# Kernel tuning notes

Measured on AMD Instinct MI355X. Metric: run time of the kernel, lower is better.

Reference implementation:

```python
import jax, jax.numpy as jnp
import numpy as np
import math

B, C, N, T = 8, 128, 256, 64  # batch, d_model, nodes, timesteps
H = 8                          # attention heads
NUM_STEPS = 50                 # diffusion steps


def _conv2d(x, w, b):
    # Conv2d with kernel (1,3), padding (0,1); x: (B,C,N,T), w: (O,I,1,3)
    y = jax.lax.conv_general_dilated(x, w, (1, 1), [(0, 0), (1, 1)],
                                     dimension_numbers=('NCHW', 'OIHW', 'NCHW'))
    return y + b[None, :, None, None]


def _linear(x, w, b=None):
    y = jnp.einsum('...i,oi->...o', x, w)
    return y if b is None else y + b


def _ln(x, g, b, eps=1e-5):
    m = jnp.mean(x, -1, keepdims=True)
    v = jnp.var(x, -1, keepdims=True)
    return (x - m) * jax.lax.rsqrt(v + eps) * g + b


def _forward(step, x, adj, wq, bq, wk, bk, w1, b1, w2, b2, theta,
             ln0_g, ln0_b, ln1_g, ln1_b, p1_w, p1_b, p2_w, p2_b,
             dxc_w, dxc_b, dec_w, dec_b, dc1_w, dc1_b, dp2_w, dp2_b):
    dk = C // H
    sq = 1.0 / math.sqrt(dk)
    sc = 1.0 / math.sqrt(C)
    # ---- normalized graph Laplacian: D^{-1/2} A D^{-1/2} (get_laplacian, normalize=True)
    d = jnp.sum(adj, -1) ** -0.5
    Lap = adj * d[:, None] * d[None, :]  # (N,N)
    # ---- temporal attention with conv-derived Q/K (MultiHeadAttentionAwareTemporal)
    q = _conv2d(x, wq, bq).reshape(B, H, dk, N, T).transpose(0, 3, 1, 4, 2)  # (B,N,H,T,dk)
    k = _conv2d(x, wk, bk).reshape(B, H, dk, N, T).transpose(0, 3, 1, 4, 2)
    v = _linear(x.transpose(0, 2, 3, 1), w1, b1).reshape(B, N, T, H, dk).transpose(0, 1, 3, 2, 4)
    p = jax.nn.softmax(jnp.einsum('bnhtd,bnhsd->bnhts', q, k) * sq, axis=-1)
    o = jnp.einsum('bnhts,bnhsd->bnhtd', p, v).transpose(0, 1, 3, 2, 4).reshape(B, N, T, C)
    xp = x.transpose(0, 2, 3, 1) + _ln(_linear(o, w2, b2), ln0_g, ln0_b)  # (B,N,T,C)
    # ---- spatial attention GCN (Spatial_Attention_layer + spatialAttentionGCN)
    xt = xp.transpose(0, 2, 1, 3)  # (B,T,N,C)
    sat = jax.nn.softmax(jnp.einsum('btnf,btmf->btnm', xt, xt) * sc, axis=-1) * sc
    y = jnp.einsum('btnm,btmf->btnf', Lap[None, None] * sat, xt)
    y = jax.nn.relu(_linear(y, theta)).transpose(0, 2, 1, 3)  # (B,N,T,C)
    h = xp + _ln(y, ln1_g, ln1_b)
    # ---- diffusion step embedding (DiffusionEmbedding)
    dim = C // 2
    freqs = 10.0 ** (jnp.arange(dim, dtype=jnp.float32) / (dim - 1) * 4.0)
    tab = jnp.arange(NUM_STEPS, dtype=jnp.float32)[:, None] * freqs[None, :]
    tab = jnp.concatenate([jnp.sin(tab), jnp.cos(tab)], -1)  # (NUM_STEPS, C)
    e = jax.nn.silu(_linear(tab[step], p1_w, p1_b))
    e = jax.nn.silu(_linear(e, p2_w, p2_b))  # (B,C)
    h = h + e[:, None, None, :]
    # ---- Decoder: conv + sigmoid-gated add + relu + 1x1 projection to 2 channels
    enc = h.transpose(0, 3, 1, 2)  # (B,C,N,T)
    xh = _conv2d(enc, dxc_w, dxc_b)
    ec = _conv2d(enc, dec_w, dec_b)
    out = jax.nn.relu(xh + jax.nn.sigmoid(ec) + _conv2d(ec, dc1_w, dc1_b))
    out = jnp.einsum('bcnt,oc->bont', out, dp2_w) + dp2_b[None, :, None, None]  # (B,2,N,T)
    return out


def setup_inputs() -> dict:
    key = jax.random.key(0)
    ks = iter(jax.random.split(key, 40))
    s = 1.0 / math.sqrt(C)
    sk = 1.0 / math.sqrt(3 * C)

    def nrm(shape, scale):
        return jax.random.normal(next(ks), shape, jnp.float32) * scale

    return {
        'x': nrm((B, C, N, T), 1.0),
        'adj': jax.random.uniform(next(ks), (N, N), jnp.float32, 0.1, 1.0),
        'step': jax.random.randint(next(ks), (B,), 0, NUM_STEPS, jnp.int32),
        'wq': nrm((C, C, 1, 3), sk), 'bq': jnp.zeros((C,), jnp.float32),
        'wk': nrm((C, C, 1, 3), sk), 'bk': jnp.zeros((C,), jnp.float32),
        'w1': nrm((C, C), s), 'b1': jnp.zeros((C,), jnp.float32),
        'w2': nrm((C, C), s), 'b2': jnp.zeros((C,), jnp.float32),
        'theta': nrm((C, C), s),
        'ln0_g': jnp.ones((C,), jnp.float32), 'ln0_b': jnp.zeros((C,), jnp.float32),
        'ln1_g': jnp.ones((C,), jnp.float32), 'ln1_b': jnp.zeros((C,), jnp.float32),
        'p1_w': nrm((C, C), s), 'p1_b': jnp.zeros((C,), jnp.float32),
        'p2_w': nrm((C, C), s), 'p2_b': jnp.zeros((C,), jnp.float32),
        'dxc_w': nrm((C, C, 1, 3), sk), 'dxc_b': jnp.zeros((C,), jnp.float32),
        'dec_w': nrm((C, C, 1, 3), sk), 'dec_b': jnp.zeros((C,), jnp.float32),
        'dc1_w': nrm((C, C, 1, 3), sk), 'dc1_b': jnp.zeros((C,), jnp.float32),
        'dp2_w': nrm((2, C), s), 'dp2_b': jnp.zeros((2,), jnp.float32),
    }


def reference(x, adj, step, wq, bq, wk, bk, w1, b1, w2, b2, theta,
              ln0_g, ln0_b, ln1_g, ln1_b, p1_w, p1_b, p2_w, p2_b,
              dxc_w, dxc_b, dec_w, dec_b, dc1_w, dc1_b, dp2_w, dp2_b):
    return _forward(step, x, adj, wq, bq, wk, bk, w1, b1, w2, b2, theta,
                    ln0_g, ln0_b, ln1_g, ln1_b, p1_w, p1_b, p2_w, p2_b,
                    dxc_w, dxc_b, dec_w, dec_b, dc1_w, dc1_b, dp2_w, dp2_b)
```

## Files before the change

### kernel.cpp

```cpp
#include <hip/hip_runtime.h>
#include <hip/hip_bf16.h>

namespace {

constexpr int C = 128, N = 256, T = 64, Bsz = 8;
constexpr int TILE = T * C;
constexpr size_t BIGE = (size_t)Bsz * N * T * C;

typedef short v8s __attribute__((ext_vector_type(8)));
typedef float v4f __attribute__((ext_vector_type(4)));

__device__ __forceinline__ float bfu(unsigned short u) {
  unsigned int x = ((unsigned int)u) << 16;
  return __uint_as_float(x);
}
__device__ __forceinline__ unsigned short f2b(float v) {
  __hip_bfloat16 h = __float2bfloat16(v);
  return *(unsigned short*)&h;
}
__device__ __forceinline__ unsigned int pk2(float a, float b) {
  return (unsigned int)f2b(a) | ((unsigned int)f2b(b) << 16);
}
__device__ __forceinline__ float ld(const void* p, size_t i, int f32) {
  if (f32) return ((const float*)p)[i];
  return bfu(((const unsigned short*)p)[i]);
}
__device__ __forceinline__ float sigm(float x) { return 1.f / (1.f + __expf(-x)); }

__global__ __launch_bounds__(64) void k_sniff(const unsigned short* x, int* flag) {
  __shared__ int cnt[64];
  int tid = threadIdx.x;
  int c = 0;
  for (int u = 0; u < 8; ++u) {
    unsigned short v = x[tid * 8 + u];
    int e = (v >> 7) & 255;
    c += (e >= 97 && e <= 157) ? 1 : 0;
  }
  cnt[tid] = c;
  __syncthreads();
  if (tid == 0) {
    int s = 0;
    for (int i = 0; i < 64; ++i) s += cnt[i];
    flag[0] = (s < 435) ? 1 : 0;
  }
}

struct PrepArgs {
  const int* flag;
  const void *wq, *wk, *w1, *w2, *th, *dxc, *dec, *dc1;
  const void *bq, *bk, *b1, *b2, *l0g, *l0b, *l1g, *l1b, *dxcb, *decb, *dc1b, *dp2w, *dp2b;
  unsigned short *wqkB, *w1B, *w2B;
  __hip_bfloat16* thB;
  unsigned short *decWb, *dxcWb, *dc1Wb;
  float *bqk, *b1f, *b2f, *l0gf, *l0bf, *l1gf, *l1bf, *dxcbf, *decbf, *dc1bf, *dp2wf, *dp2bf;
};

__global__ __launch_bounds__(256) void k_prepall(
    PrepArgs a, const void* adj, float* lap, const int* step,
    const void* p1w, const void* p1b, const void* p2w, const void* p2b, float* e) {
  __shared__ float sh[256];
  __shared__ float e1[128];
  int f = a.flag[0];
  int blk = blockIdx.x, tid = threadIdx.x;
  if (blk < 128) {
    int idx = blk * 256 + tid;
    const int stride = 32768;
    for (int i = idx; i < 256 * 384; i += stride) {
      int o = i / 384, k = i - o * 384;
      int j = k >> 7, ii = k & 127;
      float v = (o < 128) ? ld(a.wq, (o * 128 + ii) * 3 + j, f)
                          : ld(a.wk, ((o - 128) * 128 + ii) * 3 + j, f);
      a.wqkB[i] = f2b(v);
    }
    for (int i = idx; i < 16384; i += stride) {
      a.w1B[i] = f2b(ld(a.w1, i, f));
      a.w2B[i] = f2b(ld(a.w2, i, f));
      a.thB[i] = __float2bfloat16(ld(a.th, i, f));
    }
    for (int i = idx; i < 16384; i += stride) {
      int o = i >> 7, ii = i & 127;
      int sbase = (o * 128 + ii) * 3;
#pragma unroll
      for (int j = 0; j < 3; ++j) {
        int dsti = o * 384 + j * 128 + ii;
        a.decWb[dsti] = f2b(ld(a.dec, sbase + j, f));
        a.dxcWb[dsti] = f2b(ld(a.dxc, sbase + j, f));
        a.dc1Wb[dsti] = f2b(ld(a.dc1, sbase + j, f));
      }
    }
    for (int i = idx; i < 256; i += stride) {
      a.bqk[i] = (i < 128) ? ld(a.bq, i, f) : ld(a.bk, i - 128, f);
      a.dp2wf[i] = ld(a.dp2w, i, f);
    }
    for (int i = idx; i < 128; i += stride) {
      a.b1f[i] = ld(a.b1, i, f);   a.b2f[i] = ld(a.b2, i, f);
      a.l0gf[i] = ld(a.l0g, i, f); a.l0bf[i] = ld(a.l0b, i, f);
      a.l1gf[i] = ld(a.l1g, i, f); a.l1bf[i] = ld(a.l1b, i, f);
      a.dxcbf[i] = ld(a.dxcb, i, f); a.decbf[i] = ld(a.decb, i, f); a.dc1bf[i] = ld(a.dc1b, i, f);
    }
    if (idx < 2) a.dp2bf[idx] = ld(a.dp2b, idx, f);
  } else if (blk < 192) {
    float s = 0.f;
    for (int m = 0; m < 256; ++m) s += ld(adj, tid * 256 + m, f);
    sh[tid] = 1.f / sqrtf(s);
    __syncthreads();
    int n0 = (blk - 128) * 4;
    for (int idx = tid; idx < 1024; idx += 256) {
      int n = n0 + (idx >> 8), m = idx & 255;
      lap[n * 256 + m] = ld(adj, n * 256 + m, f) * sh[n] * sh[m];
    }
  } else {
    int b = blk - 192;
    if (tid < 128) {
      float sv = (float)step[b];
      int i0 = tid & 63;
      float fr = powf(10.f, (float)i0 / 63.f * 4.f);
      float ang = sv * fr;
      sh[tid] = (tid < 64) ? sinf(ang) : cosf(ang);
    }
    __syncthreads();
    if (tid < 128) {
      float aa = ld(p1b, tid, f);
      for (int i = 0; i < 128; ++i) aa += sh[i] * ld(p1w, tid * 128 + i, f);
      aa = aa * sigm(aa);
      e1[tid] = aa;
    }
    __syncthreads();
    if (tid < 128) {
      float a2 = ld(p2b, tid, f);
      for (int i = 0; i < 128; ++i) a2 += e1[i] * ld(p2w, tid * 128 + i, f);
      e[b * 128 + tid] = a2 * sigm(a2);
    }
  }
}

constexpr int XBS = 136;
constexpr int VTS = 72;

__global__ __launch_bounds__(512, 4) void k_mega1(
    const void* xin, const int* flag,
    const unsigned short* wqkB, const float* bqk,
    const unsigned short* w1B, const float* b1f,
    const unsigned short* w2B, const float* b2f,
    const float* l0g, const float* l0b, float* g0) {
  int bn = blockIdx.x, b = bn >> 8, n = bn & 255;
  __shared__ unsigned short Xb[66 * XBS];
  __shared__ unsigned short qo[64 * XBS];
  __shared__ unsigned short kls[64 * XBS];
  __shared__ unsigned short vT[128 * VTS];
  __shared__ float pS[8 * 64], pQ[8 * 64];
  __shared__ float mrow[64], vrow[64];
  int tid = threadIdx.x;
  int wv = tid >> 6, lane = tid & 63, quad = lane >> 4, lr = lane & 15;
  int f = flag[0];
  int hb = wv * 16;
  const v8s zz = {0, 0, 0, 0, 0, 0, 0, 0};
  {
    size_t xoff = (size_t)b * C * N * T + (size_t)n * T;
    const int NT = N * T;
    for (int idx = tid; idx < 1024; idx += 512) {
      int t = idx & 63, c0 = (idx >> 6) * 8;
      union { unsigned short us[8]; uint4 q; } pk;
      if (f) {
        const float* xp = (const float*)xin + xoff + (size_t)c0 * NT + t;
#pragma unroll
        for (int u = 0; u < 8; ++u) pk.us[u] = f2b(xp[(size_t)u * NT]);
      } else {
        const unsigned short* xp = (const unsigned short*)xin + xoff + (size_t)c0 * NT + t;
#pragma unroll
        for (int u = 0; u < 8; ++u) pk.us[u] = xp[(size_t)u * NT];
      }
      *(uint4*)&Xb[(t + 1) * XBS + c0] = pk.q;
    }
    if (tid < 128) { Xb[tid] = 0; Xb[65 * XBS + tid] = 0; }
  }
  __syncthreads();
  {
    int mt0 = wv * 2;
    v4f acc[2][4];
#pragma unroll
    for (int mi = 0; mi < 2; ++mi)
#pragma unroll
      for (int nt = 0; nt < 4; ++nt) acc[mi][nt] = (v4f){0.f, 0.f, 0.f, 0.f};
    for (int j = 0; j < 3; ++j) {
#pragma unroll
      for (int kt = 0; kt < 4; ++kt) {
        int ko = j * 128 + kt * 32 + quad * 8;
        v8s a0 = *(const v8s*)&wqkB[(mt0 * 16 + lr) * 384 + ko];
        v8s a1 = *(const v8s*)&wqkB[((mt0 + 1) * 16 + lr) * 384 + ko];
        int bko = kt * 32 + quad * 8;
#pragma unroll
        for (int nt = 0; nt < 4; ++nt) {
          v8s bb = *(const v8s*)&Xb[(nt * 16 + lr + j) * XBS + bko];
          acc[0][nt] = __builtin_amdgcn_mfma_f32_16x16x32_bf16(a0, bb, acc[0][nt], 0, 0, 0);
          acc[1][nt] = __builtin_amdgcn_mfma_f32_16x16x32_bf16(a1, bb, acc[1][nt], 0, 0, 0);
        }
      }
    }
    unsigned short* dst = (wv < 4) ? qo : kls;
#pragma unroll
    for (int mi = 0; mi < 2; ++mi) {
      int og = (mt0 + mi) * 16 + quad * 4;
      int oo = og & 127;
#pragma unroll
      for (int nt = 0; nt < 4; ++nt) {
        int t = nt * 16 + lr;
        *(unsigned int*)&dst[t * XBS + oo] =
            pk2(acc[mi][nt][0] + bqk[og], acc[mi][nt][1] + bqk[og + 1]);
        *(unsigned int*)&dst[t * XBS + oo + 2] =
            pk2(acc[mi][nt][2] + bqk[og + 2], acc[mi][nt][3] + bqk[og + 3]);
      }
    }
  }
  {
    v4f av[4];
#pragma unroll
    for (int nt = 0; nt < 4; ++nt) av[nt] = (v4f){0.f, 0.f, 0.f, 0.f};
#pragma unroll
    for (int kt = 0; kt < 4; ++kt) {
      int ko = kt * 32 + quad * 8;
      v8s a = *(const v8s*)&w1B[(wv * 16 + lr) * 128 + ko];
#pragma unroll
      for (int nt = 0; nt < 4; ++nt) {
        v8s bb = *(const v8s*)&Xb[(nt * 16 + lr + 1) * XBS + ko];
        av[nt] = __builtin_amdgcn_mfma_f32_16x16x32_bf16(a, bb, av[nt], 0, 0, 0);
      }
    }
#pragma unroll
    for (int nt = 0; nt < 4; ++nt) {
      int t = nt * 16 + lr;
#pragma unroll
      for (int r = 0; r < 4; ++r) {
        int o = hb + quad * 4 + r;
        vT[o * VTS + t] = f2b(av[nt][r] + b1f[o]);
      }
    }
  }
  __syncthreads();
  {
    v4f sa[4][4];
#pragma unroll
    for (int ms = 0; ms < 4; ++ms)
#pragma unroll
      for (int nt = 0; nt < 4; ++nt) sa[ms][nt] = (v4f){0.f, 0.f, 0.f, 0.f};
    {
      v8s afs[4], bfs[4];
#pragma unroll
      for (int ms = 0; ms < 4; ++ms)
        afs[ms] = (quad < 2) ? *(const v8s*)&kls[(ms * 16 + lr) * XBS + hb + quad * 8] : zz;
#pragma unroll
      for (int nt = 0; nt < 4; ++nt)
        bfs[nt] = (quad < 2) ? *(const v8s*)&qo[(nt * 16 + lr) * XBS + hb + quad * 8] : zz;
#pragma unroll
      for (int ms = 0; ms < 4; ++ms)
#pragma unroll
        for (int nt = 0; nt < 4; ++nt)
          sa[ms][nt] = __builtin_amdgcn_mfma_f32_16x16x32_bf16(afs[ms], bfs[nt], sa[ms][nt], 0, 0, 0);
    }
#pragma unroll
    for (int nt = 0; nt < 4; ++nt) {
      float mx = -1e30f;
#pragma unroll
      for (int ms = 0; ms < 4; ++ms)
#pragma unroll
        for (int r = 0; r < 4; ++r) {
          float v = sa[ms][nt][r] * 0.25f;
          sa[ms][nt][r] = v;
          mx = fmaxf(mx, v);
        }
      mx = fmaxf(mx, __shfl_xor(mx, 16, 64));
      mx = fmaxf(mx, __shfl_xor(mx, 32, 64));
      float ssum = 0.f;
#pragma unroll
      for (int ms = 0; ms < 4; ++ms)
#pragma unroll
        for (int r = 0; r < 4; ++r) {
          float e = __expf(sa[ms][nt][r] - mx);
          sa[ms][nt][r] = e;
          ssum += e;
        }
      ssum += __shfl_xor(ssum, 16, 64);
      ssum += __shfl_xor(ssum, 32, 64);
      float inv = 1.f / ssum;
#pragma unroll
      for (int ms = 0; ms < 4; ++ms)
#pragma unroll
        for (int r = 0; r < 4; ++r) sa[ms][nt][r] *= inv;
    }
    v4f ov[4];
#pragma unroll
    for (int nt = 0; nt < 4; ++nt) ov[nt] = (v4f){0.f, 0.f, 0.f, 0.f};
#pragma unroll
    for (int kt = 0; kt < 2; ++kt) {
      unsigned int pA[4][2], pB[4][2];
#pragma unroll
      for (int nt = 0; nt < 4; ++nt) {
#pragma unroll
        for (int h = 0; h < 2; ++h) {
          pA[nt][h] = pk2(sa[2 * kt][nt][2 * h], sa[2 * kt][nt][2 * h + 1]);
          pB[nt][h] = pk2(sa[2 * kt + 1][nt][2 * h], sa[2 * kt + 1][nt][2 * h + 1]);
        }
      }
      v8s aV = *(const v8s*)&vT[(hb + lr) * VTS + kt * 32 + quad * 8];
#pragma unroll
      for (int nt = 0; nt < 4; ++nt) {
        union { unsigned int u[4]; v8s s; } bu;
#pragma unroll
        for (int w = 0; w < 4; ++w) {
          int src = (2 * (quad & 1) + (w >> 1)) * 16 + lr;
          unsigned int x0 = (unsigned int)__shfl((int)pA[nt][w & 1], src, 64);
          unsigned int x1 = (unsigned int)__shfl((int)pB[nt][w & 1], src, 64);
          bu.u[w] = (quad >> 1) ? x1 : x0;
        }
        ov[nt] = __builtin_amdgcn_mfma_f32_16x16x32_bf16(aV, bu.s, ov[nt], 0, 0, 0);
      }
    }
#pragma unroll
    for (int nt = 0; nt < 4; ++nt) {
      int t = nt * 16 + lr;
      *(unsigned int*)&qo[t * XBS + hb + quad * 4] = pk2(ov[nt][0], ov[nt][1]);
      *(unsigned int*)&qo[t * XBS + hb + quad * 4 + 2] = pk2(ov[nt][2], ov[nt][3]);
    }
  }
  __syncthreads();
  v4f aw[4];
  {
#pragma unroll
    for (int nt = 0; nt < 4; ++nt) aw[nt] = (v4f){0.f, 0.f, 0.f, 0.f};
#pragma unroll
    for (int kt = 0; kt < 4; ++kt) {
      int ko = kt * 32 + quad * 8;
      v8s a = *(const v8s*)&w2B[(wv * 16 + lr) * 128 + ko];
#pragma unroll
      for (int nt = 0; nt < 4; ++nt) {
        v8s bb = *(const v8s*)&qo[(nt * 16 + lr) * XBS + ko];
        aw[nt] = __builtin_amdgcn_mfma_f32_16x16x32_bf16(a, bb, aw[nt], 0, 0, 0);
      }
    }
    int ob = hb + quad * 4;
#pragma unroll
    for (int nt = 0; nt < 4; ++nt) {
      float s = 0.f, q2 = 0.f;
#pragma unroll
      for (int r = 0; r < 4; ++r) {
        aw[nt][r] += b2f[ob + r];
        s += aw[nt][r];
        q2 += aw[nt][r] * aw[nt][r];
      }
      s += __shfl_xor(s, 16, 64);  s += __shfl_xor(s, 32, 64);
      q2 += __shfl_xor(q2, 16, 64); q2 += __shfl_xor(q2, 32, 64);
      if (quad == 0) {
        pS[wv * 64 + nt * 16 + lr] = s;
        pQ[wv * 64 + nt * 16 + lr] = q2;
      }
    }
  }
  __syncthreads();
  if (tid < 64) {
    float s = 0.f, q2 = 0.f;
#pragma unroll
    for (int w = 0; w < 8; ++w) { s += pS[w * 64 + tid]; q2 += pQ[w * 64 + tid]; }
    float mm = s * (1.f / 128.f);
    mrow[tid] = mm;
    vrow[tid] = rsqrtf(q2 * (1.f / 128.f) - mm * mm + 1e-5f);
  }
  __syncthreads();
  {
    int ob = hb + quad * 4;
    float gg[4], bb2[4];
#pragma unroll
    for (int r = 0; r < 4; ++r) { gg[r] = l0g[ob + r]; bb2[r] = l0b[ob + r]; }
    float* dst = g0 + (size_t)bn * TILE;
#pragma unroll
    for (int nt = 0; nt < 4; ++nt) {
      int t = nt * 16 + lr;
      float m = mrow[t], rs = vrow[t];
      ushort4 xr = *(const ushort4*)&Xb[(t + 1) * XBS + ob];
      float4 o4;
      o4.x = (aw[nt][0] - m) * rs * gg[0] + bb2[0] + bfu(xr.x);
      o4.y = (aw[nt][1] - m) * rs * gg[1] + bb2[1] + bfu(xr.y);
      o4.z = (aw[nt][2] - m) * rs * gg[2] + bb2[2] + bfu(xr.z);
      o4.w = (aw[nt][3] - m) * rs * gg[3] + bb2[3] + bfu(xr.w);
      *(float4*)&dst[t * 128 + ob] = o4;
    }
  }
}

constexpr int XS = 136;
constexpr int TS = 264;

__global__ __launch_bounds__(512, 1) void k_megasp(
    const float* g0, const float* lap, const unsigned short* thB,
    const float* l1g, const float* l1b, const float* e, unsigned short* g0b) {
  int bt = blockIdx.x, b = bt >> 6, t = bt & 63;
  __shared__ unsigned short R1[256 * XS];
  __shared__ unsigned short R2[256 * XS];
  __shared__ float pS[8][256], pQ[8][256];
  __shared__ float mrow[256], vrow[256];
  unsigned short* Xhi = R1;
  unsigned short* Xlo = R2;
  unsigned short* Xt = R2;
  unsigned short* Pld = R1;
  int tid = threadIdx.x;
  int wv = tid >> 6, lane = tid & 63, quad = lane >> 4, lr = lane & 15;
  int wrow0 = wv * 32;
  const float sc = 0.08838834764831845f;
  {
    size_t base = (size_t)b * (N * (size_t)TILE) + (size_t)t * 128;
    for (int idx = tid * 4; idx < 32768; idx += 2048) {
      int n = idx >> 7, c = idx & 127;
      float4 v4 = *(const float4*)&g0[base + (size_t)n * TILE + c];
      ushort4 h, l;
      h.x = f2b(v4.x); l.x = f2b(v4.x - bfu(h.x));
      h.y = f2b(v4.y); l.y = f2b(v4.y - bfu(h.y));
      h.z = f2b(v4.z); l.z = f2b(v4.z - bfu(h.z));
      h.w = f2b(v4.w); l.w = f2b(v4.w - bfu(h.w));
      *(ushort4*)&Xhi[n * XS + c] = h;
      *(ushort4*)&Xlo[n * XS + c] = l;
    }
  }
  __syncthreads();
  v4f acc[2][16];
#pragma unroll
  for (int mi = 0; mi < 2; ++mi)
#pragma unroll
    for (int nt = 0; nt < 16; ++nt) acc[mi][nt] = (v4f){0.f, 0.f, 0.f, 0.f};
  for (int kt = 0; kt < 4; ++kt) {
    int ko = kt * 32 + quad * 8;
    v8s ah0 = *(const v8s*)&Xhi[(wrow0 + lr) * XS + ko];
    v8s al0 = *(const v8s*)&Xlo[(wrow0 + lr) * XS + ko];
    v8s ah1 = *(const v8s*)&Xhi[(wrow0 + 16 + lr) * XS + ko];
    v8s al1 = *(const v8s*)&Xlo[(wrow0 + 16 + lr) * XS + ko];
#pragma unroll
    for (int nt = 0; nt < 16; ++nt) {
      v8s bh = *(const v8s*)&Xhi[(nt * 16 + lr) * XS + ko];
      v8s bl = *(const v8s*)&Xlo[(nt * 16 + lr) * XS + ko];
      acc[0][nt] = __builtin_amdgcn_mfma_f32_16x16x32_bf16(ah0, bh, acc[0][nt], 0, 0, 0);
      acc[0][nt] = __builtin_amdgcn_mfma_f32_16x16x32_bf16(ah0, bl, acc[0][nt], 0, 0, 0);
      acc[0][nt] = __builtin_amdgcn_mfma_f32_16x16x32_bf16(al0, bh, acc[0][nt], 0, 0, 0);
      acc[1][nt] = __builtin_amdgcn_mfma_f32_16x16x32_bf16(ah1, bh, acc[1][nt], 0, 0, 0);
      acc[1][nt] = __builtin_amdgcn_mfma_f32_16x16x32_bf16(ah1, bl, acc[1][nt], 0, 0, 0);
      acc[1][nt] = __builtin_amdgcn_mfma_f32_16x16x32_bf16(al1, bh, acc[1][nt], 0, 0, 0);
    }
  }
  __syncthreads();
  for (int task = tid; task < 8192; task += 512) {
    int c = task & 127, n0 = (task >> 7) * 4;
    ushort4 w;
    w.x = Xhi[(n0 + 0) * XS + c];
    w.y = Xhi[(n0 + 1) * XS + c];
    w.z = Xhi[(n0 + 2) * XS + c];
    w.w = Xhi[(n0 + 3) * XS + c];
    *(ushort4*)&Xt[c * TS + n0] = w;
  }
  __syncthreads();
  unsigned int pk1[2][8][2];
#pragma unroll
  for (int mi = 0; mi < 2; ++mi) {
#pragma unroll
    for (int r = 0; r < 4; ++r) {
      int row = wrow0 + 16 * mi + quad * 4 + r;
      float mx = -1e30f;
#pragma unroll
      for (int nt = 0; nt < 16; ++nt) {
        acc[mi][nt][r] *= sc;
        mx = fmaxf(mx, acc[mi][nt][r]);
      }
#pragma unroll
      for (int m = 8; m > 0; m >>= 1) mx = fmaxf(mx, __shfl_xor(mx, m, 16));
      float ex[16];
      float ssum = 0.f;
#pragma unroll
      for (int nt = 0; nt < 16; ++nt) { ex[nt] = __expf(acc[mi][nt][r] - mx); ssum += ex[nt]; }
#pragma unroll
      for (int m = 8; m > 0; m >>= 1) ssum += __shfl_xor(ssum, m, 16);
      float inv = sc / ssum;
      const float* lrow = lap + row * 256 + lr;
#pragma unroll
      for (int nt = 0; nt < 8; ++nt)
        Pld[row * XS + nt * 16 + lr] = f2b(ex[nt] * inv * lrow[nt * 16]);
#pragma unroll
      for (int nt = 8; nt < 16; ++nt) {
        unsigned int hbw = (unsigned int)f2b(ex[nt] * inv * lrow[nt * 16]);
        if ((r & 1) == 0) pk1[mi][nt - 8][r >> 1] = hbw;
        else pk1[mi][nt - 8][r >> 1] |= hbw << 16;
      }
    }
  }
  v4f acc2[2][8];
#pragma unroll
  for (int mi = 0; mi < 2; ++mi)
#pragma unroll
    for (int nt = 0; nt < 8; ++nt) acc2[mi][nt] = (v4f){0.f, 0.f, 0.f, 0.f};
#pragma unroll
  for (int h = 0; h < 2; ++h) {
    if (h == 1) {
#pragma unroll
      for (int mi = 0; mi < 2; ++mi) {
        int rowb = wrow0 + 16 * mi + quad * 4;
#pragma unroll
        for (int k = 0; k < 8; ++k) {
          int col = k * 16 + lr;
          unsigned int u0 = pk1[mi][k][0], u1 = pk1[mi][k][1];
          Pld[(rowb + 0) * XS + col] = (unsigned short)u0;
          Pld[(rowb + 1) * XS + col] = (unsigned short)(u0 >> 16);
          Pld[(rowb + 2) * XS + col] = (unsigned short)u1;
          Pld[(rowb + 3) * XS + col] = (unsigned short)(u1 >> 16);
        }
      }
    }
    for (int kt = 0; kt < 4; ++kt) {
      int ko = kt * 32 + quad * 8;
      v8s pa0 = *(const v8s*)&Pld[(wrow0 + lr) * XS + ko];
      v8s pa1 = *(const v8s*)&Pld[(wrow0 + 16 + lr) * XS + ko];
#pragma unroll
      for (int nt = 0; nt < 8; ++nt) {
        v8s xb = *(const v8s*)&Xt[(nt * 16 + lr) * TS + h * 128 + ko];
        acc2[0][nt] = __builtin_amdgcn_mfma_f32_16x16x32_bf16(pa0, xb, acc2[0][nt], 0, 0, 0);
        acc2[1][nt] = __builtin_amdgcn_mfma_f32_16x16x32_bf16(pa1, xb, acc2[1][nt], 0, 0, 0);
      }
    }
  }
  __syncthreads();
  unsigned short* yB = R2;
  unsigned short* ths = R1;
#pragma unroll
  for (int mi = 0; mi < 2; ++mi) {
    int nb = wrow0 + 16 * mi + quad * 4;
#pragma unroll
    for (int nt = 0; nt < 8; ++nt) {
      int c = nt * 16 + lr;
#pragma unroll
      for (int r = 0; r < 4; ++r)
        yB[(nb + r) * XS + c] = f2b(acc2[mi][nt][r]);
    }
  }
  for (int idx = tid * 8; idx < 16384; idx += 4096) {
    int o = idx >> 7, k = idx & 127;
    *(uint4*)&ths[o * 136 + k] = *(const uint4*)&thB[idx];
  }
  __syncthreads();
  v4f acc3[16];
#pragma unroll
  for (int nt = 0; nt < 16; ++nt) acc3[nt] = (v4f){0.f, 0.f, 0.f, 0.f};
#pragma unroll
  for (int kt = 0; kt < 4; ++kt) {
    int ko = kt * 32 + quad * 8;
    v8s a = *(const v8s*)&ths[(wv * 16 + lr) * 136 + ko];
#pragma unroll
    for (int nt = 0; nt < 16; ++nt) {
      v8s bb = *(const v8s*)&yB[(nt * 16 + lr) * XS + ko];
      acc3[nt] = __builtin_amdgcn_mfma_f32_16x16x32_bf16(a, bb, acc3[nt], 0, 0, 0);
    }
  }
#pragma unroll
  for (int nt = 0; nt < 16; ++nt) {
    float s = 0.f, q2 = 0.f;
#pragma unroll
    for (int r = 0; r < 4; ++r) {
      float v = fmaxf(acc3[nt][r], 0.f);
      acc3[nt][r] = v;
      s += v; q2 += v * v;
    }
    s += __shfl_xor(s, 16, 64);  s += __shfl_xor(s, 32, 64);
    q2 += __shfl_xor(q2, 16, 64); q2 += __shfl_xor(q2, 32, 64);
    if (quad == 0) { pS[wv][nt * 16 + lr] = s; pQ[wv][nt * 16 + lr] = q2; }
  }
  __syncthreads();
  if (tid < 256) {
    float s = 0.f, q2 = 0.f;
#pragma unroll
    for (int w = 0; w < 8; ++w) { s += pS[w][tid]; q2 += pQ[w][tid]; }
    float mm = s * (1.f / 128.f);
    mrow[tid] = mm;
    vrow[tid] = rsqrtf(q2 * (1.f / 128.f) - mm * mm + 1e-5f);
  }
  __syncthreads();
  {
    int o0 = wv * 16 + quad * 4;
    float gg[4], bb2[4], ev[4];
    const float* eb = e + b * 128;
#pragma unroll
    for (int r = 0; r < 4; ++r) { gg[r] = l1g[o0 + r]; bb2[r] = l1b[o0 + r]; ev[r] = eb[o0 + r]; }
#pragma unroll
    for (int nt = 0; nt < 16; ++nt) {
      int n = nt * 16 + lr;
      float m = mrow[n], rs = vrow[n];
      size_t ga = ((size_t)(b * 256 + n)) * TILE + (size_t)t * 128 + o0;
      float4 xa = *(const float4*)&g0[ga];
      ushort4 pk;
      pk.x = f2b((acc3[nt][0] - m) * rs * gg[0] + bb2[0] + xa.x + ev[0]);
      pk.y = f2b((acc3[nt][1] - m) * rs * gg[1] + bb2[1] + xa.y + ev[1]);
      pk.z = f2b((acc3[nt][2] - m) * rs * gg[2] + bb2[2] + xa.z + ev[2]);
      pk.w = f2b((acc3[nt][3] - m) * rs * gg[3] + bb2[3] + xa.w + ev[3]);
      *(ushort4*)&g0b[ga] = pk;
    }
  }
}

__global__ __launch_bounds__(512, 4) void k_megadec(
    const unsigned short* g0b, const unsigned short* decW, const float* decb,
    const unsigned short* dxcW, const float* dxcb,
    const unsigned short* dc1W, const float* dc1b,
    const float* dp2w, const float* dp2b, const int* flag, void* outv) {
  int bn = blockIdx.x, b = bn >> 8, n = bn & 255;
  int f32o = flag[0];
  __shared__ unsigned short Xm[66 * XBS];
  __shared__ unsigned short E2[66 * XBS];
  __shared__ float pb0[8][64], pb1[8][64];
  int tid = threadIdx.x;
  int wv = tid >> 6, lane = tid & 63, quad = lane >> 4, lr = lane & 15;
  int m0 = wv * 16;
  const unsigned short* gp = g0b + (size_t)bn * TILE;
  for (int idx = tid * 8; idx < TILE; idx += 4096) {
    int t = idx >> 7, c = idx & 127;
    *(uint4*)&Xm[(t + 1) * XBS + c] = *(const uint4*)&gp[idx];
  }
  if (tid < 128) {
    Xm[tid] = 0; Xm[65 * XBS + tid] = 0;
    E2[tid] = 0; E2[65 * XBS + tid] = 0;
  }
  __syncthreads();
  v4f acc[4];
  float ecv[4][4];
#pragma unroll
  for (int nt = 0; nt < 4; ++nt) acc[nt] = (v4f){0.f, 0.f, 0.f, 0.f};
  for (int j = 0; j < 3; ++j) {
#pragma unroll
    for (int kt = 0; kt < 4; ++kt) {
      v8s a = *(const v8s*)&decW[(m0 + lr) * 384 + j * 128 + kt * 32 + quad * 8];
      int bko = kt * 32 + quad * 8;
#pragma unroll
      for (int nt = 0; nt < 4; ++nt) {
        v8s bb = *(const v8s*)&Xm[(nt * 16 + lr + j) * XBS + bko];
        acc[nt] = __builtin_amdgcn_mfma_f32_16x16x32_bf16(a, bb, acc[nt], 0, 0, 0);
      }
    }
  }
#pragma unroll
  for (int nt = 0; nt < 4; ++nt) {
    int t = nt * 16 + lr;
    int o = m0 + quad * 4;
    ushort4 pk;
#pragma unroll
    for (int r = 0; r < 4; ++r) {
      float v = acc[nt][r] + decb[o + r];
      ecv[nt][r] = v;
      ((unsigned short*)&pk)[r] = f2b(v);
    }
    *(ushort4*)&E2[(t + 1) * XBS + o] = pk;
  }
  __syncthreads();
  v4f ax[4], ac[4];
#pragma unroll
  for (int nt = 0; nt < 4; ++nt) { ax[nt] = (v4f){0.f,0.f,0.f,0.f}; ac[nt] = (v4f){0.f,0.f,0.f,0.f}; }
  for (int j = 0; j < 3; ++j) {
#pragma unroll
    for (int kt = 0; kt < 4; ++kt) {
      int wo = (m0 + lr) * 384 + j * 128 + kt * 32 + quad * 8;
      v8s a1 = *(const v8s*)&dxcW[wo];
      v8s a2 = *(const v8s*)&dc1W[wo];
      int bko = kt * 32 + quad * 8;
#pragma unroll
      for (int nt = 0; nt < 4; ++nt) {
        int row = (nt * 16 + lr + j) * XBS + bko;
        v8s b1 = *(const v8s*)&Xm[row];
        v8s b2v = *(const v8s*)&E2[row];
        ax[nt] = __builtin_amdgcn_mfma_f32_16x16x32_bf16(a1, b1, ax[nt], 0, 0, 0);
        ac[nt] = __builtin_amdgcn_mfma_f32_16x16x32_bf16(a2, b2v, ac[nt], 0, 0, 0);
      }
    }
  }
#pragma unroll
  for (int nt = 0; nt < 4; ++nt) {
    float p0 = 0.f, p1 = 0.f;
#pragma unroll
    for (int r = 0; r < 4; ++r) {
      int o = m0 + quad * 4 + r;
      float v = fmaxf(ax[nt][r] + dxcb[o] + sigm(ecv[nt][r]) + ac[nt][r] + dc1b[o], 0.f);
      p0 += v * dp2w[o];
      p1 += v * dp2w[128 + o];
    }
    p0 += __shfl_xor(p0, 16, 64); p0 += __shfl_xor(p0, 32, 64);
    p1 += __shfl_xor(p1, 16, 64); p1 += __shfl_xor(p1, 32, 64);
    if (quad == 0) { pb0[wv][nt * 16 + lr] = p0; pb1[wv][nt * 16 + lr] = p1; }
  }
  __syncthreads();
  if (tid < 128) {
    int ch = tid >> 6, t = tid & 63;
    float s = 0.f;
    if (ch == 0) { for (int w = 0; w < 8; ++w) s += pb0[w][t]; s += dp2b[0]; }
    else         { for (int w = 0; w < 8; ++w) s += pb1[w][t]; s += dp2b[1]; }
    size_t oi = ((size_t)(b * 2 + ch) * 256 + n) * 64 + t;
    if (f32o) ((float*)outv)[oi] = s;
    else ((__hip_bfloat16*)outv)[oi] = __float2bfloat16(s);
  }
}

}

extern "C" void kernel_launch(void* const* d_in, const int* in_sizes, int n_in,
                              void* d_out, int out_size, void* d_ws, size_t ws_size,
                              hipStream_t stream) {
  (void)in_sizes; (void)n_in; (void)out_size; (void)ws_size;
  const void* x    = d_in[0];
  const void* adj  = d_in[1];
  const int*  step = (const int*)d_in[2];
  const void* wq   = d_in[3];
  const void* bq   = d_in[4];
  const void* wk   = d_in[5];
  const void* bk   = d_in[6];
  const void* w1   = d_in[7];
  const void* b1   = d_in[8];
  const void* w2   = d_in[9];
  const void* b2   = d_in[10];
  const void* th   = d_in[11];
  const void* l0g  = d_in[12];
  const void* l0b  = d_in[13];
  const void* l1g  = d_in[14];
  const void* l1b  = d_in[15];
  const void* p1w  = d_in[16];
  const void* p1b  = d_in[17];
  const void* p2w  = d_in[18];
  const void* p2b  = d_in[19];
  const void* dxcw = d_in[20];
  const void* dxcb = d_in[21];
  const void* decw = d_in[22];
  const void* decb = d_in[23];
  const void* dc1w = d_in[24];
  const void* dc1b = d_in[25];
  const void* dp2w = d_in[26];
  const void* dp2b = d_in[27];

  float* ws = (float*)d_ws;
  int* flag = (int*)ws;
  float* p = ws + 16;
  float* e     = p; p += 1024;
  float* lap   = p; p += 65536;
  float* wqkBv = p; p += 49152;
  float* w1Bv  = p; p += 8192;
  float* w2Bv  = p; p += 8192;
  float* thBv  = p; p += 8192;
  float* decWv = p; p += 24576;
  float* dxcWv = p; p += 24576;
  float* dc1Wv = p; p += 24576;
  float* bqk   = p; p += 256;
  float* b1f   = p; p += 128;
  float* b2f   = p; p += 128;
  float* l0gf  = p; p += 128;
  float* l0bf  = p; p += 128;
  float* l1gf  = p; p += 128;
  float* l1bf  = p; p += 128;
  float* dxcbf = p; p += 128;
  float* decbf = p; p += 128;
  float* dc1bf = p; p += 128;
  float* dp2wf = p; p += 256;
  float* dp2bf = p; p += 8;
  size_t off = (size_t)(p - ws);
  off = (off + 127) & ~(size_t)127;
  float* xf = ws + off;
  float* g0 = xf + BIGE;
  unsigned short* g0b = (unsigned short*)xf;

  PrepArgs pa;
  pa.flag = flag;
  pa.wq = wq; pa.wk = wk; pa.w1 = w1; pa.w2 = w2; pa.th = th;
  pa.dxc = dxcw; pa.dec = decw; pa.dc1 = dc1w;
  pa.bq = bq; pa.bk = bk; pa.b1 = b1; pa.b2 = b2;
  pa.l0g = l0g; pa.l0b = l0b; pa.l1g = l1g; pa.l1b = l1b;
  pa.dxcb = dxcb; pa.decb = decb; pa.dc1b = dc1b; pa.dp2w = dp2w; pa.dp2b = dp2b;
  pa.wqkB = (unsigned short*)wqkBv;
  pa.w1B = (unsigned short*)w1Bv;
  pa.w2B = (unsigned short*)w2Bv;
  pa.thB = (__hip_bfloat16*)thBv;
  pa.decWb = (unsigned short*)decWv;
  pa.dxcWb = (unsigned short*)dxcWv;
  pa.dc1Wb = (unsigned short*)dc1Wv;
  pa.bqk = bqk; pa.b1f = b1f; pa.b2f = b2f;
  pa.l0gf = l0gf; pa.l0bf = l0bf; pa.l1gf = l1gf; pa.l1bf = l1bf;
  pa.dxcbf = dxcbf; pa.decbf = decbf; pa.dc1bf = dc1bf; pa.dp2wf = dp2wf; pa.dp2bf = dp2bf;

  k_sniff<<<1, 64, 0, stream>>>((const unsigned short*)x, flag);
  k_prepall<<<200, 256, 0, stream>>>(pa, adj, lap, step, p1w, p1b, p2w, p2b, e);

  k_mega1<<<2048, 512, 0, stream>>>(x, flag, (const unsigned short*)wqkBv, bqk,
                                    (const unsigned short*)w1Bv, b1f,
                                    (const unsigned short*)w2Bv, b2f, l0gf, l0bf, g0);
  k_megasp<<<512, 512, 0, stream>>>(g0, lap, (const unsigned short*)thBv,
                                    l1gf, l1bf, e, g0b);
  k_megadec<<<2048, 512, 0, stream>>>(g0b, (const unsigned short*)decWv, decbf,
                                      (const unsigned short*)dxcWv, dxcbf,
                                      (const unsigned short*)dc1Wv, dc1bf,
                                      dp2wf, dp2bf, flag, d_out);
}
```

Before: 411.9 us.

## Move adjacency degree reduction to a separate kernel; restructure theta GEMM per-wave rows

Adds a small kernel that computes the inverse square root of each adjacency row sum with coalesced loads and warp shuffles. Previously each of 64 Laplacian blocks redundantly recomputed all 256 row sums with strided loads. In the spatial kernel, the theta GEMM is re-tiled so each wave owns 32 node rows across all 128 output channels. LayerNorm statistics can then be reduced within the wave, removing the shared-memory partial buffers and two block barriers. The cost is one extra kernel launch and more A-operand LDS loads per wave.

```diff
diff --git a/kernel.cpp b/kernel.cpp
--- a/kernel.cpp
+++ b/kernel.cpp
@@ -43,6 +43,18 @@
     for (int i = 0; i < 64; ++i) s += cnt[i];
     flag[0] = (s < 435) ? 1 : 0;
   }
+}
+
+__global__ __launch_bounds__(256) void k_dsh(const void* adj, const int* flag, float* dsh) {
+  int f = flag[0];
+  int row = blockIdx.x * 8 + (threadIdx.x >> 5);
+  int l32 = threadIdx.x & 31;
+  float s = 0.f;
+#pragma unroll
+  for (int j = 0; j < 8; ++j) s += ld(adj, (size_t)row * 256 + l32 + j * 32, f);
+#pragma unroll
+  for (int m = 16; m > 0; m >>= 1) s += __shfl_xor(s, m, 32);
+  if (l32 == 0) dsh[row] = 1.f / sqrtf(s);
 }
 
 struct PrepArgs {
@@ -56,7 +68,7 @@
 };
 
 __global__ __launch_bounds__(256) void k_prepall(
-    PrepArgs a, const void* adj, float* lap, const int* step,
+    PrepArgs a, const void* adj, const float* dsh, float* lap, const int* step,
     const void* p1w, const void* p1b, const void* p2w, const void* p2b, float* e) {
   __shared__ float sh[256];
   __shared__ float e1[128];
@@ -100,14 +112,10 @@
     }
     if (idx < 2) a.dp2bf[idx] = ld(a.dp2b, idx, f);
   } else if (blk < 192) {
-    float s = 0.f;
-    for (int m = 0; m < 256; ++m) s += ld(adj, tid * 256 + m, f);
-    sh[tid] = 1.f / sqrtf(s);
-    __syncthreads();
     int n0 = (blk - 128) * 4;
     for (int idx = tid; idx < 1024; idx += 256) {
       int n = n0 + (idx >> 8), m = idx & 255;
-      lap[n * 256 + m] = ld(adj, n * 256 + m, f) * sh[n] * sh[m];
+      lap[n * 256 + m] = ld(adj, n * 256 + m, f) * dsh[n] * dsh[m];
     }
   } else {
     int b = blk - 192;
@@ -395,8 +403,6 @@
   int bt = blockIdx.x, b = bt >> 6, t = bt & 63;
   __shared__ unsigned short R1[256 * XS];
   __shared__ unsigned short R2[256 * XS];
-  __shared__ float pS[8][256], pQ[8][256];
-  __shared__ float mrow[256], vrow[256];
   unsigned short* Xhi = R1;
   unsigned short* Xlo = R2;
   unsigned short* Xt = R2;
@@ -540,60 +546,61 @@
     *(uint4*)&ths[o * 136 + k] = *(const uint4*)&thB[idx];
   }
   __syncthreads();
-  v4f acc3[16];
-#pragma unroll
-  for (int nt = 0; nt < 16; ++nt) acc3[nt] = (v4f){0.f, 0.f, 0.f, 0.f};
+  v4f acc3[2][8];
+#pragma unroll
+  for (int nt2 = 0; nt2 < 2; ++nt2)
+#pragma unroll
+    for (int ot = 0; ot < 8; ++ot) acc3[nt2][ot] = (v4f){0.f, 0.f, 0.f, 0.f};
 #pragma unroll
   for (int kt = 0; kt < 4; ++kt) {
     int ko = kt * 32 + quad * 8;
-    v8s a = *(const v8s*)&ths[(wv * 16 + lr) * 136 + ko];
-#pragma unroll
-    for (int nt = 0; nt < 16; ++nt) {
-      v8s bb = *(const v8s*)&yB[(nt * 16 + lr) * XS + ko];
-      acc3[nt] = __builtin_amdgcn_mfma_f32_16x16x32_bf16(a, bb, acc3[nt], 0, 0, 0);
-    }
-  }
-#pragma unroll
-  for (int nt = 0; nt < 16; ++nt) {
+    v8s b0 = *(const v8s*)&yB[((wv * 2 + 0) * 16 + lr) * XS + ko];
+    v8s b1 = *(const v8s*)&yB[((wv * 2 + 1) * 16 + lr) * XS + ko];
+#pragma unroll
+    for (int ot = 0; ot < 8; ++ot) {
+      v8s a = *(const v8s*)&ths[(ot * 16 + lr) * 136 + ko];
+      acc3[0][ot] = __builtin_amdgcn_mfma_f32_16x16x32_bf16(a, b0, acc3[0][ot], 0, 0, 0);
+      acc3[1][ot] = __builtin_amdgcn_mfma_f32_16x16x32_bf16(a, b1, acc3[1][ot], 0, 0, 0);
+    }
+  }
+  float mmv[2], rrv[2];
+#pragma unroll
+  for (int nt2 = 0; nt2 < 2; ++nt2) {
     float s = 0.f, q2 = 0.f;
 #pragma unroll
-    for (int r = 0; r < 4; ++r) {
-      float v = fmaxf(acc3[nt][r], 0.f);
-      acc3[nt][r] = v;
-      s += v; q2 += v * v;
-    }
+    for (int ot = 0; ot < 8; ++ot)
+#pragma unroll
+      for (int r = 0; r < 4; ++r) {
+        float v = fmaxf(acc3[nt2][ot][r], 0.f);
+        acc3[nt2][ot][r] = v;
+        s += v; q2 += v * v;
+      }
     s += __shfl_xor(s, 16, 64);  s += __shfl_xor(s, 32, 64);
     q2 += __shfl_xor(q2, 16, 64); q2 += __shfl_xor(q2, 32, 64);
-    if (quad == 0) { pS[wv][nt * 16 + lr] = s; pQ[wv][nt * 16 + lr] = q2; }
-  }
-  __syncthreads();
-  if (tid < 256) {
-    float s = 0.f, q2 = 0.f;
-#pragma unroll
-    for (int w = 0; w < 8; ++w) { s += pS[w][tid]; q2 += pQ[w][tid]; }
-    float mm = s * (1.f / 128.f);
-    mrow[tid] = mm;
-    vrow[tid] = rsqrtf(q2 * (1.f / 128.f) - mm * mm + 1e-5f);
-  }
-  __syncthreads();
+    mmv[nt2] = s * (1.f / 128.f);
+    rrv[nt2] = rsqrtf(q2 * (1.f / 128.f) - mmv[nt2] * mmv[nt2] + 1e-5f);
+  }
   {
-    int o0 = wv * 16 + quad * 4;
-    float gg[4], bb2[4], ev[4];
     const float* eb = e + b * 128;
 #pragma unroll
-    for (int r = 0; r < 4; ++r) { gg[r] = l1g[o0 + r]; bb2[r] = l1b[o0 + r]; ev[r] = eb[o0 + r]; }
-#pragma unroll
-    for (int nt = 0; nt < 16; ++nt) {
-      int n = nt * 16 + lr;
-      float m = mrow[n], rs = vrow[n];
-      size_t ga = ((size_t)(b * 256 + n)) * TILE + (size_t)t * 128 + o0;
-      float4 xa = *(const float4*)&g0[ga];
-      ushort4 pk;
-      pk.x = f2b((acc3[nt][0] - m) * rs * gg[0] + bb2[0] + xa.x + ev[0]);
-      pk.y = f2b((acc3[nt][1] - m) * rs * gg[1] + bb2[1] + xa.y + ev[1]);
-      pk.z = f2b((acc3[nt][2] - m) * rs * gg[2] + bb2[2] + xa.z + ev[2]);
-      pk.w = f2b((acc3[nt][3] - m) * rs * gg[3] + bb2[3] + xa.w + ev[3]);
-      *(ushort4*)&g0b[ga] = pk;
+    for (int ot = 0; ot < 8; ++ot) {
+      int o0 = ot * 16 + quad * 4;
+      float gg[4], bb2[4], ev[4];
+#pragma unroll
+      for (int r = 0; r < 4; ++r) { gg[r] = l1g[o0 + r]; bb2[r] = l1b[o0 + r]; ev[r] = eb[o0 + r]; }
+#pragma unroll
+      for (int nt2 = 0; nt2 < 2; ++nt2) {
+        int n = (wv * 2 + nt2) * 16 + lr;
+        float m = mmv[nt2], rs = rrv[nt2];
+        size_t ga = ((size_t)(b * 256 + n)) * TILE + (size_t)t * 128 + o0;
+        float4 xa = *(const float4*)&g0[ga];
+        ushort4 pk;
+        pk.x = f2b((acc3[nt2][ot][0] - m) * rs * gg[0] + bb2[0] + xa.x + ev[0]);
+        pk.y = f2b((acc3[nt2][ot][1] - m) * rs * gg[1] + bb2[1] + xa.y + ev[1]);
+        pk.z = f2b((acc3[nt2][ot][2] - m) * rs * gg[2] + bb2[2] + xa.z + ev[2]);
+        pk.w = f2b((acc3[nt2][ot][3] - m) * rs * gg[3] + bb2[3] + xa.w + ev[3]);
+        *(ushort4*)&g0b[ga] = pk;
+      }
     }
   }
 }
@@ -737,6 +744,7 @@
   float* p = ws + 16;
   float* e     = p; p += 1024;
   float* lap   = p; p += 65536;
+  float* dshv  = p; p += 256;
   float* wqkBv = p; p += 49152;
   float* w1Bv  = p; p += 8192;
   float* w2Bv  = p; p += 8192;
@@ -781,7 +789,8 @@
   pa.dxcbf = dxcbf; pa.decbf = decbf; pa.dc1bf = dc1bf; pa.dp2wf = dp2wf; pa.dp2bf = dp2bf;
 
   k_sniff<<<1, 64, 0, stream>>>((const unsigned short*)x, flag);
-  k_prepall<<<200, 256, 0, stream>>>(pa, adj, lap, step, p1w, p1b, p2w, p2b, e);
+  k_dsh<<<32, 256, 0, stream>>>(adj, flag, dshv);
+  k_prepall<<<200, 256, 0, stream>>>(pa, adj, dshv, lap, step, p1w, p1b, p2w, p2b, e);
 
   k_mega1<<<2048, 512, 0, stream>>>(x, flag, (const unsigned short*)wqkBv, bqk,
                                     (const unsigned short*)w1Bv, b1f,
```

After: 406.4 us. No clear change (-1.3%).
